# Kernel optimization log

Measured on AMD Instinct MI355X. Metric: run time of the kernel, lower is better.

Reference implementation:

```python
import jax, jax.numpy as jnp
import numpy as np

# pywt db2 decomposition filters (mode='symmetric', pywt defaults)
DEC_LO = np.array([-0.12940952255092145, 0.22414386804185735,
                   0.836516303737469, 0.48296291314469025], dtype=np.float32)
DEC_HI = np.array([-0.48296291314469025, 0.836516303737469,
                   -0.22414386804185735, -0.12940952255092145], dtype=np.float32)


def _dwt_axis(x, filt, axis):
    """Single-level 1D DWT along `axis`, symmetric padding, matching pywt.

    Equivalent to: symmetric-pad by F-1 each side, full convolution with
    `filt` (true convolution => filter flipped), take indices 1,3,5,...
    Implemented as pad (F-2, F-1) + strided correlation with reversed filter.
    """
    F = filt.shape[0]
    x = jnp.moveaxis(x, axis, -1)
    N = x.shape[-1]
    out_len = (N + F - 1) // 2
    pad = [(0, 0)] * (x.ndim - 1) + [(F - 2, F - 1)]
    xp = jnp.pad(x, pad, mode='symmetric')
    filt_rev = filt[::-1]
    # sum of 4 strided slices (F=4) -- fully vectorized, no big intermediates
    out = filt_rev[0] * xp[..., 0:2 * out_len:2]
    for k in range(1, F):
        out = out + filt_rev[k] * xp[..., k:k + 2 * out_len:2]
    return jnp.moveaxis(out, -1, axis)


def setup_inputs() -> dict:
    key = jax.random.key(0)
    x = jax.random.normal(key, (16, 3, 1024, 1024), dtype=jnp.float32)
    return {"x": x}


def reference(x):
    lo = jnp.asarray(DEC_LO)
    hi = jnp.asarray(DEC_HI)
    # pywt.dwt2 -> cA = 'aa' (approx rows, approx cols),
    #              cH = 'da' (detail along axis -2, approx along axis -1)
    lo_rows = _dwt_axis(x, lo, -2)
    hi_rows = _dwt_axis(x, hi, -2)
    cA = _dwt_axis(lo_rows, lo, -1)
    cH = _dwt_axis(hi_rows, lo, -1)
    return (cA, cH)
```

## Files before the change

### kernel.cpp

```cpp
#include <hip/hip_runtime.h>


#define N 1024
#define NOUT 513
#define TI 8
#define STRIPS ((NOUT + TI - 1) / TI)

__device__ __forceinline__ int refl(int p) {
    int r = p - 2;
    r = (r < 0) ? (-1 - r) : r;
    r = (r > N - 1) ? (2 * N - 1 - r) : r;
    return r;
}

__global__ __launch_bounds__(256, 8) void dwt2_strip(const float* __restrict__ x,
                                                     float* __restrict__ out) {
    const float l0 =  0.48296291314469025f;
    const float l1 =  0.836516303737469f;
    const float l2 =  0.22414386804185735f;
    const float l3 = -0.12940952255092145f;
    const float h0 = -0.12940952255092145f;
    const float h1 = -0.22414386804185735f;
    const float h2 =  0.836516303737469f;
    const float h3 = -0.48296291314469025f;

    __shared__ float sLo[2][N];
    __shared__ float sHi[2][N];

    const int strip = blockIdx.x;
    const int img   = blockIdx.y;
    const int i0 = strip * TI;
    const int t  = threadIdx.x;
    const int c  = 4 * t;

    const float* xim = x + (size_t)img * N * N;
    const size_t plane = (size_t)NOUT * NOUT;
    float* cA = out + (size_t)img * plane;
    float* cH = out + ((size_t)48 + img) * plane;

    const int nrows = (NOUT - i0 < TI) ? (NOUT - i0) : TI;

    float4 r0 = *reinterpret_cast<const float4*>(xim + (size_t)refl(2 * i0)     * N + c);
    float4 r1 = *reinterpret_cast<const float4*>(xim + (size_t)refl(2 * i0 + 1) * N + c);
    float4 n0 = *reinterpret_cast<const float4*>(xim + (size_t)refl(2 * i0 + 2) * N + c);
    float4 n1 = *reinterpret_cast<const float4*>(xim + (size_t)refl(2 * i0 + 3) * N + c);

    for (int ii = 0; ii < nrows; ++ii) {
        const int i = i0 + ii;
        const int buf = ii & 1;

        float4 lo, hi;
        lo.x = l0 * r0.x + l1 * r1.x + l2 * n0.x + l3 * n1.x;
        lo.y = l0 * r0.y + l1 * r1.y + l2 * n0.y + l3 * n1.y;
        lo.z = l0 * r0.z + l1 * r1.z + l2 * n0.z + l3 * n1.z;
        lo.w = l0 * r0.w + l1 * r1.w + l2 * n0.w + l3 * n1.w;
        hi.x = h0 * r0.x + h1 * r1.x + h2 * n0.x + h3 * n1.x;
        hi.y = h0 * r0.y + h1 * r1.y + h2 * n0.y + h3 * n1.y;
        hi.z = h0 * r0.z + h1 * r1.z + h2 * n0.z + h3 * n1.z;
        hi.w = h0 * r0.w + h1 * r1.w + h2 * n0.w + h3 * n1.w;
        *reinterpret_cast<float4*>(&sLo[buf][c]) = lo;
        *reinterpret_cast<float4*>(&sHi[buf][c]) = hi;
        r0 = n0;
        r1 = n1;

        __syncthreads();

        if (ii + 1 < nrows) {
            const int ip = i + 1;
            n0 = *reinterpret_cast<const float4*>(xim + (size_t)refl(2 * ip + 2) * N + c);
            n1 = *reinterpret_cast<const float4*>(xim + (size_t)refl(2 * ip + 3) * N + c);
        }

        const float* __restrict__ Lrow = sLo[buf];
        const float* __restrict__ Hrow = sHi[buf];
        for (int j = t; j < NOUT; j += 256) {
            float a0, a1, a2, a3, b0, b1, b2, b3;
            if (j >= 1 && j <= NOUT - 2) {
                const int cc = 2 * j - 2;
                a0 = Lrow[cc]; a1 = Lrow[cc + 1]; a2 = Lrow[cc + 2]; a3 = Lrow[cc + 3];
                b0 = Hrow[cc]; b1 = Hrow[cc + 1]; b2 = Hrow[cc + 2]; b3 = Hrow[cc + 3];
            } else {
                const int c0 = refl(2 * j), c1 = refl(2 * j + 1);
                const int c2 = refl(2 * j + 2), c3 = refl(2 * j + 3);
                a0 = Lrow[c0]; a1 = Lrow[c1]; a2 = Lrow[c2]; a3 = Lrow[c3];
                b0 = Hrow[c0]; b1 = Hrow[c1]; b2 = Hrow[c2]; b3 = Hrow[c3];
            }
            cA[(size_t)i * NOUT + j] = l0 * a0 + l1 * a1 + l2 * a2 + l3 * a3;
            cH[(size_t)i * NOUT + j] = l0 * b0 + l1 * b1 + l2 * b2 + l3 * b3;
        }
    }
}

extern "C" void kernel_launch(void* const* d_in, const int* in_sizes, int n_in,
                              void* d_out, int out_size, void* d_ws, size_t ws_size,
                              hipStream_t stream) {
    (void)in_sizes; (void)n_in; (void)d_ws; (void)ws_size; (void)out_size;
    const float* x = (const float*)d_in[0];
    float* out = (float*)d_out;
    dim3 grid(STRIPS, 48);
    dim3 block(256);
    dwt2_strip<<<grid, block, 0, stream>>>(x, out);
}
```

Before: 314.0 us.

## Compute column DWT in registers with halo loads, removing shared memory and barriers

Each thread now handles 8 input columns and loads a 2-element halo from global memory. This lets it compute the row-filtered values and then the column-filtered outputs entirely in registers. Shared-memory staging and the per-row __syncthreads are gone, and the block shrinks to 128 threads. In exchange there are redundant halo loads, and the output stores are unaligned scalars because rows have odd length (513). Edge handling at column 0 and 512 is done with special cases.

```diff
diff --git a/kernel.cpp b/kernel.cpp
--- a/kernel.cpp
+++ b/kernel.cpp
@@ -13,7 +13,25 @@
     return r;
 }
 
-__global__ __launch_bounds__(256, 8) void dwt2_strip(const float* __restrict__ x,
+__device__ __forceinline__ float4 comb4(float w0, const float4 a, float w1, const float4 b,
+                                        float w2, const float4 c, float w3, const float4 d) {
+    float4 r;
+    r.x = fmaf(w0, a.x, fmaf(w1, b.x, fmaf(w2, c.x, w3 * d.x)));
+    r.y = fmaf(w0, a.y, fmaf(w1, b.y, fmaf(w2, c.y, w3 * d.y)));
+    r.z = fmaf(w0, a.z, fmaf(w1, b.z, fmaf(w2, c.z, w3 * d.z)));
+    r.w = fmaf(w0, a.w, fmaf(w1, b.w, fmaf(w2, c.w, w3 * d.w)));
+    return r;
+}
+
+__device__ __forceinline__ float2 comb2(float w0, const float2 a, float w1, const float2 b,
+                                        float w2, const float2 c, float w3, const float2 d) {
+    float2 r;
+    r.x = fmaf(w0, a.x, fmaf(w1, b.x, fmaf(w2, c.x, w3 * d.x)));
+    r.y = fmaf(w0, a.y, fmaf(w1, b.y, fmaf(w2, c.y, w3 * d.y)));
+    return r;
+}
+
+__global__ __launch_bounds__(128, 4) void dwt2_nolds(const float* __restrict__ x,
                                                      float* __restrict__ out) {
     const float l0 =  0.48296291314469025f;
     const float l1 =  0.836516303737469f;
@@ -24,14 +42,12 @@
     const float h2 =  0.836516303737469f;
     const float h3 = -0.48296291314469025f;
 
-    __shared__ float sLo[2][N];
-    __shared__ float sHi[2][N];
-
     const int strip = blockIdx.x;
     const int img   = blockIdx.y;
     const int i0 = strip * TI;
-    const int t  = threadIdx.x;
-    const int c  = 4 * t;
+    const int u  = threadIdx.x;
+    const int c  = 8 * u;
+    const int ce = (u == 0) ? 0 : (c - 2);
 
     const float* xim = x + (size_t)img * N * N;
     const size_t plane = (size_t)NOUT * NOUT;
@@ -40,53 +56,69 @@
 
     const int nrows = (NOUT - i0 < TI) ? (NOUT - i0) : TI;
 
-    float4 r0 = *reinterpret_cast<const float4*>(xim + (size_t)refl(2 * i0)     * N + c);
-    float4 r1 = *reinterpret_cast<const float4*>(xim + (size_t)refl(2 * i0 + 1) * N + c);
-    float4 n0 = *reinterpret_cast<const float4*>(xim + (size_t)refl(2 * i0 + 2) * N + c);
-    float4 n1 = *reinterpret_cast<const float4*>(xim + (size_t)refl(2 * i0 + 3) * N + c);
+    const float* p0 = xim + (size_t)refl(2 * i0)     * N;
+    const float* p1 = xim + (size_t)refl(2 * i0 + 1) * N;
+    const float* p2 = xim + (size_t)refl(2 * i0 + 2) * N;
+    const float* p3 = xim + (size_t)refl(2 * i0 + 3) * N;
+
+    float4 r0a = *reinterpret_cast<const float4*>(p0 + c);
+    float4 r0b = *reinterpret_cast<const float4*>(p0 + c + 4);
+    float2 r0e = *reinterpret_cast<const float2*>(p0 + ce);
+    float4 r1a = *reinterpret_cast<const float4*>(p1 + c);
+    float4 r1b = *reinterpret_cast<const float4*>(p1 + c + 4);
+    float2 r1e = *reinterpret_cast<const float2*>(p1 + ce);
+    float4 n0a = *reinterpret_cast<const float4*>(p2 + c);
+    float4 n0b = *reinterpret_cast<const float4*>(p2 + c + 4);
+    float2 n0e = *reinterpret_cast<const float2*>(p2 + ce);
+    float4 n1a = *reinterpret_cast<const float4*>(p3 + c);
+    float4 n1b = *reinterpret_cast<const float4*>(p3 + c + 4);
+    float2 n1e = *reinterpret_cast<const float2*>(p3 + ce);
 
     for (int ii = 0; ii < nrows; ++ii) {
         const int i = i0 + ii;
-        const int buf = ii & 1;
 
-        float4 lo, hi;
-        lo.x = l0 * r0.x + l1 * r1.x + l2 * n0.x + l3 * n1.x;
-        lo.y = l0 * r0.y + l1 * r1.y + l2 * n0.y + l3 * n1.y;
-        lo.z = l0 * r0.z + l1 * r1.z + l2 * n0.z + l3 * n1.z;
-        lo.w = l0 * r0.w + l1 * r1.w + l2 * n0.w + l3 * n1.w;
-        hi.x = h0 * r0.x + h1 * r1.x + h2 * n0.x + h3 * n1.x;
-        hi.y = h0 * r0.y + h1 * r1.y + h2 * n0.y + h3 * n1.y;
-        hi.z = h0 * r0.z + h1 * r1.z + h2 * n0.z + h3 * n1.z;
-        hi.w = h0 * r0.w + h1 * r1.w + h2 * n0.w + h3 * n1.w;
-        *reinterpret_cast<float4*>(&sLo[buf][c]) = lo;
-        *reinterpret_cast<float4*>(&sHi[buf][c]) = hi;
-        r0 = n0;
-        r1 = n1;
+        float4 vloA = comb4(l0, r0a, l1, r1a, l2, n0a, l3, n1a);
+        float4 vloB = comb4(l0, r0b, l1, r1b, l2, n0b, l3, n1b);
+        float2 plo  = comb2(l0, r0e, l1, r1e, l2, n0e, l3, n1e);
+        float4 vhiA = comb4(h0, r0a, h1, r1a, h2, n0a, h3, n1a);
+        float4 vhiB = comb4(h0, r0b, h1, r1b, h2, n0b, h3, n1b);
+        float2 phi  = comb2(h0, r0e, h1, r1e, h2, n0e, h3, n1e);
 
-        __syncthreads();
-
-        if (ii + 1 < nrows) {
-            const int ip = i + 1;
-            n0 = *reinterpret_cast<const float4*>(xim + (size_t)refl(2 * ip + 2) * N + c);
-            n1 = *reinterpret_cast<const float4*>(xim + (size_t)refl(2 * ip + 3) * N + c);
+        if (u == 0) {
+            plo = make_float2(vloA.y, vloA.x);
+            phi = make_float2(vhiA.y, vhiA.x);
         }
 
-        const float* __restrict__ Lrow = sLo[buf];
-        const float* __restrict__ Hrow = sHi[buf];
-        for (int j = t; j < NOUT; j += 256) {
-            float a0, a1, a2, a3, b0, b1, b2, b3;
-            if (j >= 1 && j <= NOUT - 2) {
-                const int cc = 2 * j - 2;
-                a0 = Lrow[cc]; a1 = Lrow[cc + 1]; a2 = Lrow[cc + 2]; a3 = Lrow[cc + 3];
-                b0 = Hrow[cc]; b1 = Hrow[cc + 1]; b2 = Hrow[cc + 2]; b3 = Hrow[cc + 3];
-            } else {
-                const int c0 = refl(2 * j), c1 = refl(2 * j + 1);
-                const int c2 = refl(2 * j + 2), c3 = refl(2 * j + 3);
-                a0 = Lrow[c0]; a1 = Lrow[c1]; a2 = Lrow[c2]; a3 = Lrow[c3];
-                b0 = Hrow[c0]; b1 = Hrow[c1]; b2 = Hrow[c2]; b3 = Hrow[c3];
-            }
-            cA[(size_t)i * NOUT + j] = l0 * a0 + l1 * a1 + l2 * a2 + l3 * a3;
-            cH[(size_t)i * NOUT + j] = l0 * b0 + l1 * b1 + l2 * b2 + l3 * b3;
+        r0a = n0a; r0b = n0b; r0e = n0e;
+        r1a = n1a; r1b = n1b; r1e = n1e;
+        if (ii + 1 < nrows) {
+            const float* q0 = xim + (size_t)refl(2 * i + 4) * N;
+            const float* q1 = xim + (size_t)refl(2 * i + 5) * N;
+            n0a = *reinterpret_cast<const float4*>(q0 + c);
+            n0b = *reinterpret_cast<const float4*>(q0 + c + 4);
+            n0e = *reinterpret_cast<const float2*>(q0 + ce);
+            n1a = *reinterpret_cast<const float4*>(q1 + c);
+            n1b = *reinterpret_cast<const float4*>(q1 + c + 4);
+            n1e = *reinterpret_cast<const float2*>(q1 + ce);
+        }
+
+        float oA0 = fmaf(l0, plo.x,  fmaf(l1, plo.y,  fmaf(l2, vloA.x, l3 * vloA.y)));
+        float oA1 = fmaf(l0, vloA.x, fmaf(l1, vloA.y, fmaf(l2, vloA.z, l3 * vloA.w)));
+        float oA2 = fmaf(l0, vloA.z, fmaf(l1, vloA.w, fmaf(l2, vloB.x, l3 * vloB.y)));
+        float oA3 = fmaf(l0, vloB.x, fmaf(l1, vloB.y, fmaf(l2, vloB.z, l3 * vloB.w)));
+        float oH0 = fmaf(l0, phi.x,  fmaf(l1, phi.y,  fmaf(l2, vhiA.x, l3 * vhiA.y)));
+        float oH1 = fmaf(l0, vhiA.x, fmaf(l1, vhiA.y, fmaf(l2, vhiA.z, l3 * vhiA.w)));
+        float oH2 = fmaf(l0, vhiA.z, fmaf(l1, vhiA.w, fmaf(l2, vhiB.x, l3 * vhiB.y)));
+        float oH3 = fmaf(l0, vhiB.x, fmaf(l1, vhiB.y, fmaf(l2, vhiB.z, l3 * vhiB.w)));
+
+        float* pa = cA + (size_t)i * NOUT + 4 * u;
+        float* ph = cH + (size_t)i * NOUT + 4 * u;
+        pa[0] = oA0; pa[1] = oA1; pa[2] = oA2; pa[3] = oA3;
+        ph[0] = oH0; ph[1] = oH1; ph[2] = oH2; ph[3] = oH3;
+
+        if (u == 127) {
+            pa[4] = fmaf(l0, vloB.z, fmaf(l1, vloB.w, fmaf(l2, vloB.w, l3 * vloB.z)));
+            ph[4] = fmaf(l0, vhiB.z, fmaf(l1, vhiB.w, fmaf(l2, vhiB.w, l3 * vhiB.z)));
         }
     }
 }
@@ -98,6 +130,6 @@
     const float* x = (const float*)d_in[0];
     float* out = (float*)d_out;
     dim3 grid(STRIPS, 48);
-    dim3 block(256);
-    dwt2_strip<<<grid, block, 0, stream>>>(x, out);
+    dim3 block(128);
+    dwt2_nolds<<<grid, block, 0, stream>>>(x, out);
 }
```

New measurement: 316.0 us. About the same (+0.6%).
